# Kernel tuning notes

Measured on AMD Instinct MI355X. Metric: run time of the kernel, lower is better.

The kernel has to match this reference:

```python
import jax, jax.numpy as jnp
import numpy as np

P_SCALAR = 40.0
NEG_INF = -1e30


def setup_inputs() -> dict:
    key = jax.random.key(0)
    k1, k2, k3, k4, k5 = jax.random.split(key, 5)
    B, Dk, Dv, T, H, W = 8, 128, 512, 2, 56, 56
    qkey = jax.random.normal(k1, (B, Dk, H, W), dtype=jnp.float32)
    qmask = jax.random.randint(k2, (B, 1, H, W), 0, 2).astype(jnp.bool_)
    mkey = jax.random.normal(k3, (B, Dk, T, H, W), dtype=jnp.float32)
    mval = jax.random.normal(k4, (B, Dv, T, H, W), dtype=jnp.float32)
    mmask = jax.random.randint(k5, (B, 1, T, H, W), 0, 2).astype(jnp.bool_)
    return {"qkey": qkey, "qmask": qmask, "mkey": mkey, "mval": mval, "mmask": mmask}


def reference(qkey, qmask, mkey, mval, mmask):
    # Faithful vectorized version of SegmentationAttentionSeparateModule.maskRead.
    # Torch loops over b, gathers masked query/memory columns, does
    # softmax(p_scalar * mk^T qk, dim=0) then mv @ p, scattering into zeros.
    # Equivalent dense math: masked softmax over memory positions, and zero
    # output at query positions outside qmask.
    B, Dk, H, W = qkey.shape
    Dv = mval.shape[1]
    M = H * W                       # query positions
    qk = qkey.reshape(B, Dk, M)     # [B, Dk, M]
    mk = mkey.reshape(B, Dk, -1)    # [B, Dk, N], N = T*H*W
    mv = mval.reshape(B, Dv, -1)    # [B, Dv, N]
    qm = qmask.reshape(B, 1, M)     # [B, 1, M]
    mm = mmask.reshape(B, -1)       # [B, N]

    # scores over memory (axis 1) per query column, p_scalar * mk^T qk
    scores = P_SCALAR * jnp.einsum('bdn,bdm->bnm', mk, qk)       # [B, N, M]
    scores = jnp.where(mm[:, :, None], scores, NEG_INF)
    p = jax.nn.softmax(scores, axis=1)                           # softmax over memory
    p = jnp.where(mm[:, :, None], p, 0.0)                        # guard all-masked rows
    qread = jnp.einsum('bdn,bnm->bdm', mv, p)                    # [B, Dv, M]
    qread = jnp.where(qm, qread, 0.0)                            # only masked query cols
    return qread.reshape(B, Dv, H, W)
```

## Files before the change

### kernel.cpp

```cpp
#include <hip/hip_runtime.h>
#include <stdint.h>

#define B_    8
#define DK_   128
#define DV_   512
#define M_    3136
#define N_    6272
#define MT128_ 25
#define NSEG_ 8
#define TH_   30.0f
#define MARGIN_ 36.0f
#define BKT_  64

typedef short bf16x8 __attribute__((ext_vector_type(8)));
typedef float f32x16 __attribute__((ext_vector_type(16)));
typedef unsigned short u16x8 __attribute__((ext_vector_type(8)));

__device__ __forceinline__ unsigned fkey(float x) {
  unsigned u = __float_as_uint(x);
  return (u & 0x80000000u) ? ~u : (u | 0x80000000u);
}
__device__ __forceinline__ float fdec(unsigned k) {
  return __uint_as_float((k & 0x80000000u) ? (k & 0x7fffffffu) : ~k);
}
__device__ __forceinline__ unsigned short f2bf(float x) {
  unsigned u = __float_as_uint(x);
  return (unsigned short)((u + 0x7fffu + ((u >> 16) & 1u)) >> 16);
}
__device__ __forceinline__ float bf2f(unsigned short h) {
  return __uint_as_float(((unsigned)h) << 16);
}

__global__ __launch_bounds__(256)
void scan_masks(const int* __restrict__ qmask, const int* __restrict__ mmask,
                int* __restrict__ qlist, int* __restrict__ nlist,
                int* __restrict__ qcnt, int* __restrict__ ncnt) {
  int b = blockIdx.x;
  int tid = threadIdx.x, lane = tid & 63, wv = tid >> 6;
  __shared__ int wsum[4];
  __shared__ int cbase;
  if (tid == 0) cbase = 0;
  __syncthreads();
  const int* src = (blockIdx.y == 0) ? (qmask + b * M_) : (mmask + b * N_);
  int* dst = (blockIdx.y == 0) ? (qlist + b * M_) : (nlist + b * N_);
  int len = (blockIdx.y == 0) ? M_ : N_;
  for (int base = 0; base < len; base += 256) {
    int i = base + tid;
    int flag = (i < len) ? (src[i] != 0) : 0;
    unsigned long long bal = __ballot(flag);
    int prefix = __popcll(bal & ((1ull << lane) - 1ull));
    if (lane == 0) wsum[wv] = __popcll(bal);
    __syncthreads();
    int woff = 0;
    for (int t = 0; t < wv; ++t) woff += wsum[t];
    int total = wsum[0] + wsum[1] + wsum[2] + wsum[3];
    if (flag) dst[cbase + woff + prefix] = i;
    __syncthreads();
    if (tid == 0) cbase += total;
    __syncthreads();
  }
  if (tid == 0) {
    if (blockIdx.y == 0) qcnt[b] = cbase; else ncnt[b] = cbase;
  }
}

__global__ __launch_bounds__(256)
void transpose_key(const float* __restrict__ src, float* __restrict__ dstf,
                   unsigned short* __restrict__ dstb, int X, float scale) {
  __shared__ float T[64][65];
  int b = blockIdx.z, dt = blockIdx.y, xt = blockIdx.x;
  int lane = threadIdx.x & 63, ri = threadIdx.x >> 6;
  #pragma unroll
  for (int k = 0; k < 16; ++k) {
    int dl = ri * 16 + k;
    T[dl][lane] = src[((size_t)b * DK_ + dt * 64 + dl) * X + xt * 64 + lane];
  }
  __syncthreads();
  #pragma unroll
  for (int k = 0; k < 16; ++k) {
    int xl = ri * 16 + k;
    float v = scale * T[lane][xl];
    size_t idx = ((size_t)b * X + xt * 64 + xl) * DK_ + dt * 64 + lane;
    dstf[idx] = v;
    dstb[idx] = f2bf(v);
  }
}

__global__ __launch_bounds__(256)
void transpose_val(const float* __restrict__ mval, unsigned short* __restrict__ mvalT) {
  __shared__ float T[64][65];
  int b = blockIdx.z, dvt = blockIdx.y, nt = blockIdx.x;
  int lane = threadIdx.x & 63, ri = threadIdx.x >> 6;
  #pragma unroll
  for (int k = 0; k < 16; ++k) {
    int dvl = ri * 16 + k;
    T[dvl][lane] = mval[((size_t)b * DV_ + dvt * 64 + dvl) * N_ + nt * 64 + lane];
  }
  __syncthreads();
  #pragma unroll
  for (int k = 0; k < 16; ++k) {
    int nl = ri * 16 + k;
    mvalT[((size_t)b * N_ + nt * 64 + nl) * DV_ + dvt * 64 + lane] = f2bf(T[lane][nl]);
  }
}

__global__ __launch_bounds__(256, 3)
void score_mfma(const unsigned short* __restrict__ qkb, const unsigned short* __restrict__ mkb,
                const int* __restrict__ qlist, const int* __restrict__ nlist,
                const int* __restrict__ qcnt, const int* __restrict__ ncnt,
                unsigned* __restrict__ maxkey, unsigned* __restrict__ bcnt,
                unsigned* __restrict__ bucket) {
  int bid = blockIdx.x;
  int seg = bid & (NSEG_ - 1);
  int t   = bid >> 3;
  int mt  = t % MT128_;
  int b   = t / MT128_;
  int mc = qcnt[b];
  if (mt * 128 >= mc) return;
  int nc = ncnt[b];
  int ntiles = (nc + 63) >> 6;
  int t0 = (ntiles * seg) / NSEG_;
  int t1 = (ntiles * (seg + 1)) / NSEG_;
  if (t0 >= t1) return;

  __shared__ unsigned short Qs[128 * 128];
  __shared__ unsigned short Ks[64 * 128];
  __shared__ int Morig[128];
  __shared__ int NorigBuf[2][64];
  __shared__ unsigned runkey[128];
  char* Qsb = (char*)Qs;
  char* Ksb = (char*)Ks;

  int tid = threadIdx.x;
  int lane = tid & 63, wv = tid >> 6;
  int l31 = lane & 31, lhi = lane >> 5;
  int mrow = wv * 32 + l31;

  for (int i = tid; i < 2048; i += 256) {
    int row = i >> 4, ck = i & 15;
    int cm = mt * 128 + row;
    int col = (cm < mc) ? qlist[b * M_ + cm] : qlist[b * M_];
    if (ck == 0) Morig[row] = (cm < mc) ? col : -1;
    uint4 v = *(const uint4*)&qkb[((size_t)b * M_ + col) * DK_ + ck * 8];
    *(uint4*)(Qsb + (row << 8) + ((ck ^ (row & 7)) << 4)) = v;
  }
  if (tid < 128) runkey[tid] = 0u;
  __syncthreads();

  int qswz = (mrow & 7) << 4;
  int kswz = (l31 & 7) << 4;

  for (int tt = t0; tt < t1; ++tt) {
    int nbase = tt << 6;
    int par = tt & 1;
    for (int i = tid; i < 1024; i += 256) {
      int row = i >> 4, ck = i & 15;
      int jn = nbase + row;
      int ncol = (jn < nc) ? nlist[b * N_ + jn] : nlist[b * N_];
      if (ck == 0) NorigBuf[par][row] = (jn < nc) ? ncol : -1;
      uint4 v = *(const uint4*)&mkb[((size_t)b * N_ + ncol) * DK_ + ck * 8];
      *(uint4*)(Ksb + (row << 8) + ((ck ^ (row & 7)) << 4)) = v;
    }
    __syncthreads();

    f32x16 acc0, acc1;
    #pragma unroll
    for (int r = 0; r < 16; ++r) { acc0[r] = 0.0f; acc1[r] = 0.0f; }
    #pragma unroll
    for (int kc = 0; kc < 8; ++kc) {
      int koff = (kc << 5) | (lhi << 4);
      bf16x8 bq = *(const bf16x8*)(Qsb + (mrow << 8) + (koff ^ qswz));
      bf16x8 a0 = *(const bf16x8*)(Ksb + (l31 << 8) + (koff ^ kswz));
      bf16x8 a1 = *(const bf16x8*)(Ksb + ((32 + l31) << 8) + (koff ^ kswz));
      acc0 = __builtin_amdgcn_mfma_f32_32x32x16_bf16(a0, bq, acc0, 0, 0, 0);
      acc1 = __builtin_amdgcn_mfma_f32_32x32x16_bf16(a1, bq, acc1, 0, 0, 0);
    }

    float cmx = fmaxf(acc0[0], acc1[0]);
    #pragma unroll
    for (int r = 1; r < 16; ++r) cmx = fmaxf(cmx, fmaxf(acc0[r], acc1[r]));
    cmx = fmaxf(cmx, __shfl_xor(cmx, 32));
    if (lane < 32) {
      unsigned k = fkey(cmx);
      if (k > runkey[mrow]) runkey[mrow] = k;
    }
    __syncthreads();
    if (tid < 128 && Morig[tid] >= 0) {
      unsigned mine = runkey[tid];
      unsigned old = atomicMax(&maxkey[b * M_ + Morig[tid]], mine);
      if (old > mine) runkey[tid] = old;
    }
    __syncthreads();
    {
      int mo = Morig[mrow];
      if (mo >= 0) {
        float thr = fdec(runkey[mrow]) - MARGIN_;
        #pragma unroll
        for (int r = 0; r < 16; ++r) {
          if (acc0[r] >= thr) {
            int nl = (r & 3) + ((r >> 2) << 3) + (lhi << 2);
            int no = NorigBuf[par][nl];
            if (no >= 0) {
              unsigned slot = atomicAdd(&bcnt[b * M_ + mo], 1u);
              if (slot < (unsigned)BKT_)
                bucket[(((size_t)(b * M_ + mo)) << 6) + slot] = (unsigned)no;
            }
          }
          if (acc1[r] >= thr) {
            int nl = 32 + (r & 3) + ((r >> 2) << 3) + (lhi << 2);
            int no = NorigBuf[par][nl];
            if (no >= 0) {
              unsigned slot = atomicAdd(&bcnt[b * M_ + mo], 1u);
              if (slot < (unsigned)BKT_)
                bucket[(((size_t)(b * M_ + mo)) << 6) + slot] = (unsigned)no;
            }
          }
        }
      }
    }
    __syncthreads();
  }
}

__device__ __forceinline__ float dot128(const float* __restrict__ q,
                                        const float* __restrict__ k) {
  float s = 0.f;
  #pragma unroll 8
  for (int i = 0; i < DK_; i += 4) {
    float4 a = *(const float4*)&q[i];
    float4 bb = *(const float4*)&k[i];
    s += a.x * bb.x + a.y * bb.y + a.z * bb.z + a.w * bb.w;
  }
  return s;
}

__global__ __launch_bounds__(256)
void pv_exact(const float* __restrict__ qkeyT, const float* __restrict__ mkeyT,
              const unsigned short* __restrict__ mvalT,
              const int* __restrict__ qlist, const int* __restrict__ qcnt,
              const int* __restrict__ nlist, const int* __restrict__ ncnt,
              const unsigned* __restrict__ bcnt, const unsigned* __restrict__ bucket,
              unsigned short* __restrict__ outT) {
  int b = blockIdx.y;
  int wv = threadIdx.x >> 6, lane = threadIdx.x & 63;
  int c = blockIdx.x * 4 + wv;
  if (c >= qcnt[b]) return;
  int m = qlist[b * M_ + c];
  unsigned cnt = bcnt[b * M_ + m];
  const float* qrow = qkeyT + ((size_t)b * M_ + m) * DK_;
  float acc[8] = {0.f, 0.f, 0.f, 0.f, 0.f, 0.f, 0.f, 0.f};
  float lsum = 0.f;

  if (cnt <= (unsigned)BKT_) {
    int n = -1;
    if (lane < (int)cnt) n = (int)bucket[(((size_t)(b * M_ + m)) << 6) + lane];
    float sv = -3.0e38f;
    if (n >= 0) sv = dot128(qrow, mkeyT + ((size_t)b * N_ + n) * DK_);
    float mx = sv;
    #pragma unroll
    for (int o = 32; o > 0; o >>= 1) mx = fmaxf(mx, __shfl_xor(mx, o));
    float e = (n >= 0 && sv >= mx - TH_) ? expf(sv - mx) : 0.f;
    lsum = e;
    #pragma unroll
    for (int o = 32; o > 0; o >>= 1) lsum += __shfl_xor(lsum, o);
    unsigned long long alive = __ballot(e > 0.f);
    while (alive) {
      int lb = __ffsll((unsigned long long)alive) - 1;
      alive &= alive - 1;
      float w = __shfl(e, lb);
      int nn = __shfl(n, lb);
      u16x8 vvv = *(const u16x8*)(mvalT + ((size_t)b * N_ + nn) * DV_ + lane * 8);
      #pragma unroll
      for (int r = 0; r < 8; ++r) acc[r] += w * bf2f(vvv[r]);
    }
  } else {
    int nc = ncnt[b];
    float mx = -3.0e38f;
    for (int base = 0; base < nc; base += 64) {
      int jn = base + lane;
      float sv = -3.0e38f;
      if (jn < nc) {
        int n = nlist[b * N_ + jn];
        sv = dot128(qrow, mkeyT + ((size_t)b * N_ + n) * DK_);
      }
      mx = fmaxf(mx, sv);
    }
    #pragma unroll
    for (int o = 32; o > 0; o >>= 1) mx = fmaxf(mx, __shfl_xor(mx, o));
    for (int base = 0; base < nc; base += 64) {
      int jn = base + lane;
      int n = -1;
      float sv = -3.0e38f;
      if (jn < nc) {
        n = nlist[b * N_ + jn];
        sv = dot128(qrow, mkeyT + ((size_t)b * N_ + n) * DK_);
      }
      float e = (n >= 0 && sv >= mx - TH_) ? expf(sv - mx) : 0.f;
      lsum += e;
      unsigned long long alive = __ballot(e > 0.f);
      while (alive) {
        int lb = __ffsll((unsigned long long)alive) - 1;
        alive &= alive - 1;
        float w = __shfl(e, lb);
        int nn = __shfl(n, lb);
        u16x8 vvv = *(const u16x8*)(mvalT + ((size_t)b * N_ + nn) * DV_ + lane * 8);
        #pragma unroll
        for (int r = 0; r < 8; ++r) acc[r] += w * bf2f(vvv[r]);
      }
    }
    #pragma unroll
    for (int o = 32; o > 0; o >>= 1) lsum += __shfl_xor(lsum, o);
  }

  float inv = (lsum > 0.f) ? 1.0f / lsum : 0.0f;
  u16x8 ov;
  #pragma unroll
  for (int r = 0; r < 8; ++r) ov[r] = f2bf(acc[r] * inv);
  *(u16x8*)(outT + ((size_t)b * M_ + m) * DV_ + lane * 8) = ov;
}

__global__ __launch_bounds__(256)
void finalize_T(const unsigned short* __restrict__ outT, const int* __restrict__ qmask,
                float* __restrict__ out) {
  __shared__ float T[64][65];
  int b = blockIdx.z, dvt = blockIdx.y, mt = blockIdx.x;
  int lane = threadIdx.x & 63, ri = threadIdx.x >> 6;
  #pragma unroll
  for (int k = 0; k < 16; ++k) {
    int ml = ri * 16 + k;
    int m = mt * 64 + ml;
    bool act = (qmask[b * M_ + m] != 0);
    T[ml][lane] = act ? bf2f(outT[((size_t)b * M_ + m) * DV_ + dvt * 64 + lane]) : 0.f;
  }
  __syncthreads();
  #pragma unroll
  for (int k = 0; k < 16; ++k) {
    int dvl = ri * 16 + k;
    out[((size_t)b * DV_ + dvt * 64 + dvl) * M_ + mt * 64 + lane] = T[lane][dvl];
  }
}

extern "C" void kernel_launch(void* const* d_in, const int* in_sizes, int n_in,
                              void* d_out, int out_size, void* d_ws, size_t ws_size,
                              hipStream_t stream) {
  const float* qkey  = (const float*)d_in[0];
  const int*   qmask = (const int*)d_in[1];
  const float* mkey  = (const float*)d_in[2];
  const float* mval  = (const float*)d_in[3];
  const int*   mmask = (const int*)d_in[4];
  float* out = (float*)d_out;

  uint8_t* w = (uint8_t*)d_ws;
  unsigned*       maxkey = (unsigned*)(w + 0);
  unsigned*       bcnt   = (unsigned*)(w + 100352);
  int*            qcnt   = (int*)(w + 200704);
  int*            ncnt   = (int*)(w + 200736);
  int*            qlist  = (int*)(w + 200832);
  int*            nlist  = (int*)(w + 301184);
  unsigned*       bucket = (unsigned*)(w + 501888);
  float*          qkeyT  = (float*)(w + 6924416);
  float*          mkeyT  = (float*)(w + 19769472);
  unsigned short* qkb    = (unsigned short*)(w + 45459584);
  unsigned short* mkb    = (unsigned short*)(w + 51882112);
  unsigned short* outTb  = (unsigned short*)(w + 64727168);
  unsigned short* mvalT  = (unsigned short*)(w + 90417280);

  hipMemsetAsync(d_ws, 0, 200832, stream);

  scan_masks<<<dim3(B_, 2), 256, 0, stream>>>(qmask, mmask, qlist, nlist, qcnt, ncnt);
  transpose_key<<<dim3(M_ / 64, DK_ / 64, B_), 256, 0, stream>>>(qkey, qkeyT, qkb, M_, 40.0f);
  transpose_key<<<dim3(N_ / 64, DK_ / 64, B_), 256, 0, stream>>>(mkey, mkeyT, mkb, N_, 1.0f);
  transpose_val<<<dim3(N_ / 64, DV_ / 64, B_), 256, 0, stream>>>(mval, mvalT);

  score_mfma<<<B_ * MT128_ * NSEG_, 256, 0, stream>>>(
      qkb, mkb, qlist, nlist, qcnt, ncnt, maxkey, bcnt, bucket);

  pv_exact<<<dim3((M_ + 3) / 4, B_), 256, 0, stream>>>(
      qkeyT, mkeyT, mvalT, qlist, qcnt, nlist, ncnt, bcnt, bucket, outTb);

  finalize_T<<<dim3(M_ / 64, DV_ / 64, B_), 256, 0, stream>>>(outTb, qmask, out);
}
```

Measured before the change: 212.2 us.

## Fuse prep kernels, drop memory-mask compaction, double-buffer key tiles via direct LDS loads

Merges the mask scan, the three transposes and the workspace memset into a single prep kernel, removing several launches. The score kernel no longer compacts memory positions; it walks all dense N tiles and applies mmask through ballot bits. It keeps the query fragments in registers instead of LDS and double-buffers key tiles with global_load_lds, with fewer block barriers and occupancy raised to 4. The pv fallback also iterates the dense N range with mask checks. The cost is extra MFMA work on masked-out memory columns, which roughly doubles score compute, in exchange for less gather overhead and better overlap.

```diff
diff --git a/kernel.cpp b/kernel.cpp
--- a/kernel.cpp
+++ b/kernel.cpp
@@ -8,6 +8,7 @@
 #define N_    6272
 #define MT128_ 25
 #define NSEG_ 8
+#define NTILES_ 98
 #define TH_   30.0f
 #define MARGIN_ 36.0f
 #define BKT_  64
@@ -32,82 +33,97 @@
 }
 
 __global__ __launch_bounds__(256)
-void scan_masks(const int* __restrict__ qmask, const int* __restrict__ mmask,
-                int* __restrict__ qlist, int* __restrict__ nlist,
-                int* __restrict__ qcnt, int* __restrict__ ncnt) {
-  int b = blockIdx.x;
-  int tid = threadIdx.x, lane = tid & 63, wv = tid >> 6;
-  __shared__ int wsum[4];
-  __shared__ int cbase;
-  if (tid == 0) cbase = 0;
-  __syncthreads();
-  const int* src = (blockIdx.y == 0) ? (qmask + b * M_) : (mmask + b * N_);
-  int* dst = (blockIdx.y == 0) ? (qlist + b * M_) : (nlist + b * N_);
-  int len = (blockIdx.y == 0) ? M_ : N_;
-  for (int base = 0; base < len; base += 256) {
-    int i = base + tid;
-    int flag = (i < len) ? (src[i] != 0) : 0;
-    unsigned long long bal = __ballot(flag);
-    int prefix = __popcll(bal & ((1ull << lane) - 1ull));
-    if (lane == 0) wsum[wv] = __popcll(bal);
-    __syncthreads();
-    int woff = 0;
-    for (int t = 0; t < wv; ++t) woff += wsum[t];
-    int total = wsum[0] + wsum[1] + wsum[2] + wsum[3];
-    if (flag) dst[cbase + woff + prefix] = i;
-    __syncthreads();
-    if (tid == 0) cbase += total;
-    __syncthreads();
-  }
-  if (tid == 0) {
-    if (blockIdx.y == 0) qcnt[b] = cbase; else ncnt[b] = cbase;
-  }
-}
-
-__global__ __launch_bounds__(256)
-void transpose_key(const float* __restrict__ src, float* __restrict__ dstf,
-                   unsigned short* __restrict__ dstb, int X, float scale) {
+void prep_kernel(const float* __restrict__ qkey, const int* __restrict__ qmask,
+                 const float* __restrict__ mkey, const float* __restrict__ mval,
+                 float* __restrict__ qkeyT, unsigned short* __restrict__ qkb,
+                 float* __restrict__ mkeyT, unsigned short* __restrict__ mkb,
+                 unsigned short* __restrict__ mvalT,
+                 int* __restrict__ qlist, int* __restrict__ qcnt,
+                 unsigned* __restrict__ zbase) {
   __shared__ float T[64][65];
-  int b = blockIdx.z, dt = blockIdx.y, xt = blockIdx.x;
+  int r = blockIdx.x;
   int lane = threadIdx.x & 63, ri = threadIdx.x >> 6;
-  #pragma unroll
-  for (int k = 0; k < 16; ++k) {
-    int dl = ri * 16 + k;
-    T[dl][lane] = src[((size_t)b * DK_ + dt * 64 + dl) * X + xt * 64 + lane];
-  }
-  __syncthreads();
-  #pragma unroll
-  for (int k = 0; k < 16; ++k) {
-    int xl = ri * 16 + k;
-    float v = scale * T[lane][xl];
-    size_t idx = ((size_t)b * X + xt * 64 + xl) * DK_ + dt * 64 + lane;
-    dstf[idx] = v;
-    dstb[idx] = f2bf(v);
-  }
-}
-
-__global__ __launch_bounds__(256)
-void transpose_val(const float* __restrict__ mval, unsigned short* __restrict__ mvalT) {
-  __shared__ float T[64][65];
-  int b = blockIdx.z, dvt = blockIdx.y, nt = blockIdx.x;
-  int lane = threadIdx.x & 63, ri = threadIdx.x >> 6;
-  #pragma unroll
-  for (int k = 0; k < 16; ++k) {
-    int dvl = ri * 16 + k;
-    T[dvl][lane] = mval[((size_t)b * DV_ + dvt * 64 + dvl) * N_ + nt * 64 + lane];
-  }
-  __syncthreads();
-  #pragma unroll
-  for (int k = 0; k < 16; ++k) {
-    int nl = ri * 16 + k;
-    mvalT[((size_t)b * N_ + nt * 64 + nl) * DV_ + dvt * 64 + lane] = f2bf(T[lane][nl]);
-  }
-}
-
-__global__ __launch_bounds__(256, 3)
+  if (r < 784) {
+    int xt = r % 49, dt = (r / 49) & 1, b = r / 98;
+    #pragma unroll
+    for (int k = 0; k < 16; ++k) {
+      int dl = ri * 16 + k;
+      T[dl][lane] = qkey[((size_t)b * DK_ + dt * 64 + dl) * M_ + xt * 64 + lane];
+    }
+    __syncthreads();
+    #pragma unroll
+    for (int k = 0; k < 16; ++k) {
+      int xl = ri * 16 + k;
+      float v = 40.0f * T[lane][xl];
+      size_t idx = ((size_t)b * M_ + xt * 64 + xl) * DK_ + dt * 64 + lane;
+      qkeyT[idx] = v;
+      qkb[idx] = f2bf(v);
+    }
+  } else if (r < 2352) {
+    int r2 = r - 784;
+    int xt = r2 % 98, dt = (r2 / 98) & 1, b = r2 / 196;
+    #pragma unroll
+    for (int k = 0; k < 16; ++k) {
+      int dl = ri * 16 + k;
+      T[dl][lane] = mkey[((size_t)b * DK_ + dt * 64 + dl) * N_ + xt * 64 + lane];
+    }
+    __syncthreads();
+    #pragma unroll
+    for (int k = 0; k < 16; ++k) {
+      int xl = ri * 16 + k;
+      float v = T[lane][xl];
+      size_t idx = ((size_t)b * N_ + xt * 64 + xl) * DK_ + dt * 64 + lane;
+      mkeyT[idx] = v;
+      mkb[idx] = f2bf(v);
+    }
+  } else if (r < 8624) {
+    int r3 = r - 2352;
+    int nt = r3 % 98, dvt = (r3 / 98) & 7, b = r3 / 784;
+    #pragma unroll
+    for (int k = 0; k < 16; ++k) {
+      int dvl = ri * 16 + k;
+      T[dvl][lane] = mval[((size_t)b * DV_ + dvt * 64 + dvl) * N_ + nt * 64 + lane];
+    }
+    __syncthreads();
+    #pragma unroll
+    for (int k = 0; k < 16; ++k) {
+      int nl = ri * 16 + k;
+      mvalT[((size_t)b * N_ + nt * 64 + nl) * DV_ + dvt * 64 + lane] = f2bf(T[lane][nl]);
+    }
+  } else if (r < 8632) {
+    int b = r - 8624;
+    __shared__ int wsum[4];
+    __shared__ int cbase;
+    int tid = threadIdx.x, wv = tid >> 6;
+    if (tid == 0) cbase = 0;
+    __syncthreads();
+    for (int base = 0; base < M_; base += 256) {
+      int i = base + tid;
+      int flag = (i < M_) ? (qmask[b * M_ + i] != 0) : 0;
+      unsigned long long bal = __ballot(flag);
+      int prefix = __popcll(bal & ((1ull << lane) - 1ull));
+      if (lane == 0) wsum[wv] = __popcll(bal);
+      __syncthreads();
+      int woff = 0;
+      for (int t = 0; t < wv; ++t) woff += wsum[t];
+      int total = wsum[0] + wsum[1] + wsum[2] + wsum[3];
+      if (flag) qlist[b * M_ + cbase + woff + prefix] = i;
+      __syncthreads();
+      if (tid == 0) cbase += total;
+      __syncthreads();
+    }
+    if (tid == 0) qcnt[b] = cbase;
+  } else {
+    int z = r - 8632;
+    unsigned* p = zbase + z * 1024;
+    for (int i = threadIdx.x; i < 1024; i += 256) p[i] = 0u;
+  }
+}
+
+__global__ __launch_bounds__(256, 4)
 void score_mfma(const unsigned short* __restrict__ qkb, const unsigned short* __restrict__ mkb,
-                const int* __restrict__ qlist, const int* __restrict__ nlist,
-                const int* __restrict__ qcnt, const int* __restrict__ ncnt,
+                const int* __restrict__ qlist, const int* __restrict__ qcnt,
+                const int* __restrict__ mmask,
                 unsigned* __restrict__ maxkey, unsigned* __restrict__ bcnt,
                 unsigned* __restrict__ bucket) {
   int bid = blockIdx.x;
@@ -117,107 +133,113 @@
   int b   = t / MT128_;
   int mc = qcnt[b];
   if (mt * 128 >= mc) return;
-  int nc = ncnt[b];
-  int ntiles = (nc + 63) >> 6;
-  int t0 = (ntiles * seg) / NSEG_;
-  int t1 = (ntiles * (seg + 1)) / NSEG_;
-  if (t0 >= t1) return;
-
-  __shared__ unsigned short Qs[128 * 128];
-  __shared__ unsigned short Ks[64 * 128];
-  __shared__ int Morig[128];
-  __shared__ int NorigBuf[2][64];
-  __shared__ unsigned runkey[128];
-  char* Qsb = (char*)Qs;
-  char* Ksb = (char*)Ks;
+  int t0 = (NTILES_ * seg) / NSEG_;
+  int t1 = (NTILES_ * (seg + 1)) / NSEG_;
+
+  __shared__ unsigned short Ks[2][64 * 128];
 
   int tid = threadIdx.x;
   int lane = tid & 63, wv = tid >> 6;
   int l31 = lane & 31, lhi = lane >> 5;
   int mrow = wv * 32 + l31;
 
-  for (int i = tid; i < 2048; i += 256) {
-    int row = i >> 4, ck = i & 15;
-    int cm = mt * 128 + row;
-    int col = (cm < mc) ? qlist[b * M_ + cm] : qlist[b * M_];
-    if (ck == 0) Morig[row] = (cm < mc) ? col : -1;
-    uint4 v = *(const uint4*)&qkb[((size_t)b * M_ + col) * DK_ + ck * 8];
-    *(uint4*)(Qsb + (row << 8) + ((ck ^ (row & 7)) << 4)) = v;
-  }
-  if (tid < 128) runkey[tid] = 0u;
+  int cm = mt * 128 + mrow;
+  int col = (cm < mc) ? qlist[b * M_ + cm] : qlist[b * M_];
+  int mo  = (cm < mc) ? col : -1;
+  const unsigned short* qrow = qkb + ((size_t)b * M_ + col) * DK_;
+  bf16x8 qf[8];
+  #pragma unroll
+  for (int kc = 0; kc < 8; ++kc)
+    qf[kc] = *(const bf16x8*)(qrow + (kc * 2 + lhi) * 8);
+
+  const unsigned short* mkb_b = mkb + (size_t)b * N_ * DK_;
+  const int* mm_b = mmask + b * N_;
+
+  {
+    int nbase = t0 << 6;
+    char* kd = (char*)&Ks[0][0];
+    #pragma unroll
+    for (int i = 0; i < 4; ++i) {
+      int c = wv * 4 + i;
+      const unsigned short* src = mkb_b + ((size_t)(nbase + lane)) * DK_ + c * 8;
+      __builtin_amdgcn_global_load_lds(
+          (const __attribute__((address_space(1))) unsigned*)src,
+          (__attribute__((address_space(3))) unsigned*)(kd + c * 1024), 16, 0, 0);
+    }
+  }
+  asm volatile("s_waitcnt vmcnt(0)" ::: "memory");
   __syncthreads();
 
-  int qswz = (mrow & 7) << 4;
-  int kswz = (l31 & 7) << 4;
+  float runmax = -3.0e38f;
 
   for (int tt = t0; tt < t1; ++tt) {
+    int cur = (tt - t0) & 1;
     int nbase = tt << 6;
-    int par = tt & 1;
-    for (int i = tid; i < 1024; i += 256) {
-      int row = i >> 4, ck = i & 15;
-      int jn = nbase + row;
-      int ncol = (jn < nc) ? nlist[b * N_ + jn] : nlist[b * N_];
-      if (ck == 0) NorigBuf[par][row] = (jn < nc) ? ncol : -1;
-      uint4 v = *(const uint4*)&mkb[((size_t)b * N_ + ncol) * DK_ + ck * 8];
-      *(uint4*)(Ksb + (row << 8) + ((ck ^ (row & 7)) << 4)) = v;
-    }
-    __syncthreads();
-
+    if (tt + 1 < t1) {
+      int nb2 = (tt + 1) << 6;
+      char* kd = (char*)&Ks[cur ^ 1][0];
+      #pragma unroll
+      for (int i = 0; i < 4; ++i) {
+        int c = wv * 4 + i;
+        const unsigned short* src = mkb_b + ((size_t)(nb2 + lane)) * DK_ + c * 8;
+        __builtin_amdgcn_global_load_lds(
+            (const __attribute__((address_space(1))) unsigned*)src,
+            (__attribute__((address_space(3))) unsigned*)(kd + c * 1024), 16, 0, 0);
+      }
+    }
+    unsigned long long bits = __ballot(mm_b[nbase + lane] != 0);
+
+    const char* kb = (const char*)&Ks[cur][0];
     f32x16 acc0, acc1;
     #pragma unroll
-    for (int r = 0; r < 16; ++r) { acc0[r] = 0.0f; acc1[r] = 0.0f; }
+    for (int r = 0; r < 16; ++r) { acc0[r] = 0.f; acc1[r] = 0.f; }
     #pragma unroll
     for (int kc = 0; kc < 8; ++kc) {
-      int koff = (kc << 5) | (lhi << 4);
-      bf16x8 bq = *(const bf16x8*)(Qsb + (mrow << 8) + (koff ^ qswz));
-      bf16x8 a0 = *(const bf16x8*)(Ksb + (l31 << 8) + (koff ^ kswz));
-      bf16x8 a1 = *(const bf16x8*)(Ksb + ((32 + l31) << 8) + (koff ^ kswz));
-      acc0 = __builtin_amdgcn_mfma_f32_32x32x16_bf16(a0, bq, acc0, 0, 0, 0);
-      acc1 = __builtin_amdgcn_mfma_f32_32x32x16_bf16(a1, bq, acc1, 0, 0, 0);
-    }
-
-    float cmx = fmaxf(acc0[0], acc1[0]);
-    #pragma unroll
-    for (int r = 1; r < 16; ++r) cmx = fmaxf(cmx, fmaxf(acc0[r], acc1[r]));
+      int c = kc * 2 + lhi;
+      bf16x8 a0 = *(const bf16x8*)(kb + c * 1024 + l31 * 16);
+      bf16x8 a1 = *(const bf16x8*)(kb + c * 1024 + (32 + l31) * 16);
+      acc0 = __builtin_amdgcn_mfma_f32_32x32x16_bf16(a0, qf[kc], acc0, 0, 0, 0);
+      acc1 = __builtin_amdgcn_mfma_f32_32x32x16_bf16(a1, qf[kc], acc1, 0, 0, 0);
+    }
+
+    unsigned long long b0 = bits >> (lhi << 2);
+    unsigned long long b1 = (bits >> 32) >> (lhi << 2);
+    float cmx = -3.0e38f;
+    #pragma unroll
+    for (int r = 0; r < 16; ++r) {
+      const int pos = (r & 3) + ((r >> 2) << 3);
+      if ((b0 >> pos) & 1) cmx = fmaxf(cmx, acc0[r]);
+      if ((b1 >> pos) & 1) cmx = fmaxf(cmx, acc1[r]);
+    }
     cmx = fmaxf(cmx, __shfl_xor(cmx, 32));
-    if (lane < 32) {
-      unsigned k = fkey(cmx);
-      if (k > runkey[mrow]) runkey[mrow] = k;
-    }
-    __syncthreads();
-    if (tid < 128 && Morig[tid] >= 0) {
-      unsigned mine = runkey[tid];
-      unsigned old = atomicMax(&maxkey[b * M_ + Morig[tid]], mine);
-      if (old > mine) runkey[tid] = old;
-    }
-    __syncthreads();
-    {
-      int mo = Morig[mrow];
-      if (mo >= 0) {
-        float thr = fdec(runkey[mrow]) - MARGIN_;
-        #pragma unroll
-        for (int r = 0; r < 16; ++r) {
-          if (acc0[r] >= thr) {
-            int nl = (r & 3) + ((r >> 2) << 3) + (lhi << 2);
-            int no = NorigBuf[par][nl];
-            if (no >= 0) {
-              unsigned slot = atomicAdd(&bcnt[b * M_ + mo], 1u);
-              if (slot < (unsigned)BKT_)
-                bucket[(((size_t)(b * M_ + mo)) << 6) + slot] = (unsigned)no;
-            }
-          }
-          if (acc1[r] >= thr) {
-            int nl = 32 + (r & 3) + ((r >> 2) << 3) + (lhi << 2);
-            int no = NorigBuf[par][nl];
-            if (no >= 0) {
-              unsigned slot = atomicAdd(&bcnt[b * M_ + mo], 1u);
-              if (slot < (unsigned)BKT_)
-                bucket[(((size_t)(b * M_ + mo)) << 6) + slot] = (unsigned)no;
-            }
-          }
+    runmax = fmaxf(runmax, cmx);
+
+    unsigned old = 0u;
+    if (lhi == 0 && mo >= 0) old = atomicMax(&maxkey[b * M_ + mo], fkey(runmax));
+
+    if (mo >= 0) {
+      float thr = runmax - MARGIN_;
+      #pragma unroll
+      for (int r = 0; r < 16; ++r) {
+        const int pos = (r & 3) + ((r >> 2) << 3);
+        if (((b0 >> pos) & 1) && acc0[r] >= thr) {
+          unsigned slot = atomicAdd(&bcnt[b * M_ + mo], 1u);
+          if (slot < (unsigned)BKT_)
+            bucket[(((size_t)(b * M_ + mo)) << 6) + slot] =
+                (unsigned)(nbase + pos + (lhi << 2));
+        }
+        if (((b1 >> pos) & 1) && acc1[r] >= thr) {
+          unsigned slot = atomicAdd(&bcnt[b * M_ + mo], 1u);
+          if (slot < (unsigned)BKT_)
+            bucket[(((size_t)(b * M_ + mo)) << 6) + slot] =
+                (unsigned)(nbase + 32 + pos + (lhi << 2));
         }
       }
     }
+    if (lhi == 0) runmax = fmaxf(runmax, fdec(old));
+    runmax = __shfl(runmax, l31);
+
+    asm volatile("s_waitcnt vmcnt(0)" ::: "memory");
     __syncthreads();
   }
 }
@@ -238,7 +260,7 @@
 void pv_exact(const float* __restrict__ qkeyT, const float* __restrict__ mkeyT,
               const unsigned short* __restrict__ mvalT,
               const int* __restrict__ qlist, const int* __restrict__ qcnt,
-              const int* __restrict__ nlist, const int* __restrict__ ncnt,
+              const int* __restrict__ mmask,
               const unsigned* __restrict__ bcnt, const unsigned* __restrict__ bucket,
               unsigned short* __restrict__ outT) {
   int b = blockIdx.y;
@@ -274,28 +296,22 @@
       for (int r = 0; r < 8; ++r) acc[r] += w * bf2f(vvv[r]);
     }
   } else {
-    int nc = ncnt[b];
     float mx = -3.0e38f;
-    for (int base = 0; base < nc; base += 64) {
-      int jn = base + lane;
+    for (int base = 0; base < N_; base += 64) {
+      int n = base + lane;
       float sv = -3.0e38f;
-      if (jn < nc) {
-        int n = nlist[b * N_ + jn];
+      if (mmask[b * N_ + n] != 0)
         sv = dot128(qrow, mkeyT + ((size_t)b * N_ + n) * DK_);
-      }
       mx = fmaxf(mx, sv);
     }
     #pragma unroll
     for (int o = 32; o > 0; o >>= 1) mx = fmaxf(mx, __shfl_xor(mx, o));
-    for (int base = 0; base < nc; base += 64) {
-      int jn = base + lane;
-      int n = -1;
+    for (int base = 0; base < N_; base += 64) {
+      int n = base + lane;
+      bool act = (mmask[b * N_ + n] != 0);
       float sv = -3.0e38f;
-      if (jn < nc) {
-        n = nlist[b * N_ + jn];
-        sv = dot128(qrow, mkeyT + ((size_t)b * N_ + n) * DK_);
-      }
-      float e = (n >= 0 && sv >= mx - TH_) ? expf(sv - mx) : 0.f;
+      if (act) sv = dot128(qrow, mkeyT + ((size_t)b * N_ + n) * DK_);
+      float e = (act && sv >= mx - TH_) ? expf(sv - mx) : 0.f;
       lsum += e;
       unsigned long long alive = __ballot(e > 0.f);
       while (alive) {
@@ -354,29 +370,24 @@
   unsigned*       maxkey = (unsigned*)(w + 0);
   unsigned*       bcnt   = (unsigned*)(w + 100352);
   int*            qcnt   = (int*)(w + 200704);
-  int*            ncnt   = (int*)(w + 200736);
   int*            qlist  = (int*)(w + 200832);
-  int*            nlist  = (int*)(w + 301184);
-  unsigned*       bucket = (unsigned*)(w + 501888);
-  float*          qkeyT  = (float*)(w + 6924416);
-  float*          mkeyT  = (float*)(w + 19769472);
-  unsigned short* qkb    = (unsigned short*)(w + 45459584);
-  unsigned short* mkb    = (unsigned short*)(w + 51882112);
-  unsigned short* outTb  = (unsigned short*)(w + 64727168);
-  unsigned short* mvalT  = (unsigned short*)(w + 90417280);
-
-  hipMemsetAsync(d_ws, 0, 200832, stream);
-
-  scan_masks<<<dim3(B_, 2), 256, 0, stream>>>(qmask, mmask, qlist, nlist, qcnt, ncnt);
-  transpose_key<<<dim3(M_ / 64, DK_ / 64, B_), 256, 0, stream>>>(qkey, qkeyT, qkb, M_, 40.0f);
-  transpose_key<<<dim3(N_ / 64, DK_ / 64, B_), 256, 0, stream>>>(mkey, mkeyT, mkb, N_, 1.0f);
-  transpose_val<<<dim3(N_ / 64, DV_ / 64, B_), 256, 0, stream>>>(mval, mvalT);
+  unsigned*       bucket = (unsigned*)(w + 301184);
+  float*          qkeyT  = (float*)(w + 6723712);
+  float*          mkeyT  = (float*)(w + 19568768);
+  unsigned short* qkb    = (unsigned short*)(w + 45258880);
+  unsigned short* mkb    = (unsigned short*)(w + 51681408);
+  unsigned short* outTb  = (unsigned short*)(w + 64526464);
+  unsigned short* mvalT  = (unsigned short*)(w + 90216576);
+
+  prep_kernel<<<8681, 256, 0, stream>>>(qkey, qmask, mkey, mval,
+                                        qkeyT, qkb, mkeyT, mkb, mvalT,
+                                        qlist, qcnt, maxkey );
 
   score_mfma<<<B_ * MT128_ * NSEG_, 256, 0, stream>>>(
-      qkb, mkb, qlist, nlist, qcnt, ncnt, maxkey, bcnt, bucket);
-
-  pv_exact<<<dim3((M_ + 3) / 4, B_), 256, 0, stream>>>(
-      qkeyT, mkeyT, mvalT, qlist, qcnt, nlist, ncnt, bcnt, bucket, outTb);
+      qkb, mkb, qlist, qcnt, mmask, maxkey, bcnt, bucket);
+
+  pv_exact<<<dim3(M_ / 4, B_), 256, 0, stream>>>(
+      qkeyT, mkeyT, mvalT, qlist, qcnt, mmask, bcnt, bucket, outTb);
 
   finalize_T<<<dim3(M_ / 64, DV_ / 64, B_), 256, 0, stream>>>(outTb, qmask, out);
 }
```

Result: faster. 186.8 us (-12.0%).
